# Optimization experiments

Hardware: AMD Instinct MI355X
Metric: run time of the kernel (lower is better)

The kernel has to match this reference:

```python
import jax, jax.numpy as jnp
import numpy as np

B, C, K, H, W = 64, 512, 64, 64, 64
EPS = 1e-12  # torch F.normalize eps


def setup_inputs() -> dict:
    key = jax.random.key(0)
    k1, k2, k3, k4 = jax.random.split(key, 4)
    x = jax.random.normal(k1, (B, C, H, W), dtype=jnp.float32)
    conv_w = jax.random.normal(k2, (K, C), dtype=jnp.float32) * 0.1  # 1x1 conv weight, squeezed
    conv_b = jax.random.normal(k3, (K,), dtype=jnp.float32) * 0.1
    centroids = jax.random.normal(k4, (K, C), dtype=jnp.float32)
    return {"x": x, "conv_w": conv_w, "conv_b": conv_b, "centroids": centroids}


def _l2norm(v, axis):
    n = jnp.sqrt(jnp.sum(v * v, axis=axis, keepdims=True))
    return v / jnp.maximum(n, EPS)


def reference(x, conv_w, conv_b, centroids):
    b, c, h, w = x.shape
    k = centroids.shape[0]
    hw = h * w
    # F.normalize(x, p=2, dim=1)
    xn = _l2norm(x, axis=1)
    # 1x1 conv -> [b,k,h,w] -> [b,k,hw], softmax over clusters
    logits = jnp.einsum('bchw,kc->bkhw', xn, conv_w) + conv_b[None, :, None, None]
    soft_assign = jax.nn.softmax(logits.reshape(b, k, hw), axis=1)
    # faithful to original: x.view(b, -1, c) with NO permute (channel-major reinterpretation)
    x_flatten = xn.reshape(b, hw, c)
    # vlad[b,k,c] = sum_i a[b,k,i] * (xf[b,i,c] - cent[k,c])
    vlad = (jnp.einsum('bki,bic->bkc', soft_assign, x_flatten)
            - jnp.sum(soft_assign, axis=2)[:, :, None] * centroids[None])
    vlad = _l2norm(vlad, axis=2)            # intra-normalize per cluster
    vlad = vlad.reshape(b, -1)
    vlad = _l2norm(vlad, axis=1)            # global L2 normalize
    return vlad
```

## Files before the change

kernel.cpp:

```cpp
#include <hip/hip_runtime.h>

#define HW 4096
#define NC 512
#define NK 64
#define NB 64

typedef unsigned short u16;
typedef float  float4v __attribute__((ext_vector_type(4)));
typedef short  short8  __attribute__((ext_vector_type(8)));

__device__ __forceinline__ u16 f2bf(float f){
  unsigned u = __builtin_bit_cast(unsigned, f);
  u += 0x7fffu + ((u >> 16) & 1u);
  return (u16)(u >> 16);
}
__device__ __forceinline__ unsigned pk2(float a, float b){
  return (unsigned)f2bf(a) | ((unsigned)f2bf(b) << 16);
}

__global__ __launch_bounds__(256) void nv_k1(
    const float* __restrict__ x, const float* __restrict__ w,
    const float* __restrict__ bias, float* __restrict__ invnorm,
    u16* __restrict__ a_out, float* __restrict__ asum)
{
  __shared__ u16 w_sh[NK * 40];
  __shared__ u16 x_sh[256 * 40];
  __shared__ float bias_sh[NK];

  const int t    = threadIdx.x;
  const int b    = blockIdx.y;
  const int p0   = blockIdx.x * 256;
  const int wave = t >> 6, lane = t & 63, q = lane >> 4, l16 = lane & 15;

  if (t < NK) bias_sh[t] = bias[t];

  const float* xb = x + (size_t)b * NC * HW;
  float sumsq = 0.f;

  float4v acc[4][4];
  const float4v zf = {0.f, 0.f, 0.f, 0.f};
  #pragma unroll
  for (int i = 0; i < 4; ++i)
    #pragma unroll
    for (int j = 0; j < 4; ++j) acc[i][j] = zf;

  for (int step = 0; step < 16; ++step){
    const int c0 = step * 32;
    __syncthreads();
    {
      const int m = t >> 2, cq = (t & 3) * 8;
      const float* wp = w + m * NC + c0 + cq;
      float4 w0 = *(const float4*)wp;
      float4 w1 = *(const float4*)(wp + 4);
      uint4 pk;
      pk.x = pk2(w0.x, w0.y); pk.y = pk2(w0.z, w0.w);
      pk.z = pk2(w1.x, w1.y); pk.w = pk2(w1.z, w1.w);
      *(uint4*)&w_sh[m * 40 + cq] = pk;
    }
    {
      const float* xp = xb + (size_t)c0 * HW + p0 + t;
      #pragma unroll
      for (int c8 = 0; c8 < 4; ++c8){
        float v0 = xp[(c8*8+0)*HW], v1 = xp[(c8*8+1)*HW];
        float v2 = xp[(c8*8+2)*HW], v3 = xp[(c8*8+3)*HW];
        float v4 = xp[(c8*8+4)*HW], v5 = xp[(c8*8+5)*HW];
        float v6 = xp[(c8*8+6)*HW], v7 = xp[(c8*8+7)*HW];
        sumsq += v0*v0 + v1*v1 + v2*v2 + v3*v3 + v4*v4 + v5*v5 + v6*v6 + v7*v7;
        uint4 pk;
        pk.x = pk2(v0, v1); pk.y = pk2(v2, v3);
        pk.z = pk2(v4, v5); pk.w = pk2(v6, v7);
        *(uint4*)&x_sh[t * 40 + c8 * 8] = pk;
      }
    }
    __syncthreads();
    short8 av[4], bv[4];
    #pragma unroll
    for (int ms = 0; ms < 4; ++ms)
      av[ms] = *(const short8*)&w_sh[(ms*16 + l16) * 40 + q*8];
    #pragma unroll
    for (int ns = 0; ns < 4; ++ns)
      bv[ns] = *(const short8*)&x_sh[(wave*64 + ns*16 + l16) * 40 + q*8];
    #pragma unroll
    for (int ms = 0; ms < 4; ++ms)
      #pragma unroll
      for (int ns = 0; ns < 4; ++ns)
        acc[ms][ns] = __builtin_amdgcn_mfma_f32_16x16x32_bf16(av[ms], bv[ns], acc[ms][ns], 0, 0, 0);
  }

  float inv = 1.f / fmaxf(sqrtf(sumsq), 1e-12f);
  invnorm[(size_t)b * HW + p0 + t] = inv;

  float inv_n[4];
  #pragma unroll
  for (int ns = 0; ns < 4; ++ns) inv_n[ns] = __shfl(inv, ns*16 + l16, 64);

  #pragma unroll
  for (int ns = 0; ns < 4; ++ns){
    float mx = -3.4e38f;
    #pragma unroll
    for (int ms = 0; ms < 4; ++ms)
      #pragma unroll
      for (int r = 0; r < 4; ++r){
        float lv = fmaf(acc[ms][ns][r], inv_n[ns], bias_sh[ms*16 + q*4 + r]);
        acc[ms][ns][r] = lv;
        mx = fmaxf(mx, lv);
      }
    mx = fmaxf(mx, __shfl_xor(mx, 16, 64));
    mx = fmaxf(mx, __shfl_xor(mx, 32, 64));
    float s = 0.f;
    #pragma unroll
    for (int ms = 0; ms < 4; ++ms)
      #pragma unroll
      for (int r = 0; r < 4; ++r){
        float e = __expf(acc[ms][ns][r] - mx);
        acc[ms][ns][r] = e;
        s += e;
      }
    s += __shfl_xor(s, 16, 64);
    s += __shfl_xor(s, 32, 64);
    float is = 1.f / s;
    #pragma unroll
    for (int ms = 0; ms < 4; ++ms)
      #pragma unroll
      for (int r = 0; r < 4; ++r) acc[ms][ns][r] *= is;
  }

  u16* ap = a_out + (size_t)b * NK * HW + p0 + wave * 64;
  #pragma unroll
  for (int ms = 0; ms < 4; ++ms)
    #pragma unroll
    for (int r = 0; r < 4; ++r){
      const int m = ms*16 + q*4 + r;
      #pragma unroll
      for (int ns = 0; ns < 4; ++ns)
        ap[(size_t)m * HW + ns*16 + l16] = f2bf(acc[ms][ns][r]);
    }

  #pragma unroll
  for (int ms = 0; ms < 4; ++ms)
    #pragma unroll
    for (int r = 0; r < 4; ++r){
      const int m = ms*16 + q*4 + r;
      float s = acc[ms][0][r] + acc[ms][1][r] + acc[ms][2][r] + acc[ms][3][r];
      s += __shfl_xor(s, 1, 64); s += __shfl_xor(s, 2, 64);
      s += __shfl_xor(s, 4, 64); s += __shfl_xor(s, 8, 64);
      if (l16 == 0) atomicAdd(&asum[b * NK + m], s);
    }
}

__global__ __launch_bounds__(256) void nv_k2(
    const float* __restrict__ x, const u16* __restrict__ a_buf,
    const float* __restrict__ invnorm, const float* __restrict__ asum,
    const float* __restrict__ cent, float* __restrict__ vlad)
{
  __shared__ u16 a_sh[NK * 40];
  __shared__ u16 x_sh[32 * 132];
  __shared__ float inv_sh[8 * 128];
  __shared__ float asum_sh[NK];

  const int t    = threadIdx.x;
  const int b    = blockIdx.y;
  const int cc0  = blockIdx.x * 128;
  const int wave = t >> 6, lane = t & 63, q = lane >> 4, l16 = lane & 15;

  {
    const int r = t >> 5, ccl = (t & 31) * 4;
    *(float4*)&inv_sh[r * 128 + ccl] =
        *(const float4*)&invnorm[(size_t)b * HW + r * NC + cc0 + ccl];
  }
  if (t < NK) asum_sh[t] = asum[b * NK + t];
  __syncthreads();

  const int il = t >> 5, cc_off = (t & 31) * 4;
  const float4 iv = *(const float4*)&inv_sh[il * 128 + cc_off];

  const float* xb = x + (size_t)b * NC * HW;
  const u16*   ab = a_buf + (size_t)b * NK * HW;

  float4v acc[4][2];
  const float4v zf = {0.f, 0.f, 0.f, 0.f};
  #pragma unroll
  for (int i = 0; i < 4; ++i){ acc[i][0] = zf; acc[i][1] = zf; }

  for (int step = 0; step < 128; ++step){
    const int i0 = step * 32;
    __syncthreads();
    {
      const int k = t >> 2, iq = (t & 3) * 8;
      *(float4*)&a_sh[k * 40 + iq] = *(const float4*)&ab[(size_t)k * HW + i0 + iq];
    }
    #pragma unroll
    for (int rr = 0; rr < 4; ++rr){
      const int i = i0 + il + rr * 8;
      const float* xp = xb + (size_t)i * NC + cc0 + cc_off;
      float4 xv = *(const float4*)xp;
      uint2 pk;
      pk.x = pk2(xv.x * iv.x, xv.y * iv.y);
      pk.y = pk2(xv.z * iv.z, xv.w * iv.w);
      *(uint2*)&x_sh[(il + rr * 8) * 132 + cc_off] = pk;
    }
    __syncthreads();
    short8 av[4];
    #pragma unroll
    for (int ms = 0; ms < 4; ++ms)
      av[ms] = *(const short8*)&a_sh[(ms*16 + l16) * 40 + q*8];
    #pragma unroll
    for (int ns = 0; ns < 2; ++ns){
      const int nn = wave * 32 + ns * 16 + l16;
      short8 bv;
      #pragma unroll
      for (int j = 0; j < 8; ++j)
        bv[j] = (short)x_sh[(q*8 + j) * 132 + nn];
      #pragma unroll
      for (int ms = 0; ms < 4; ++ms)
        acc[ms][ns] = __builtin_amdgcn_mfma_f32_16x16x32_bf16(av[ms], bv, acc[ms][ns], 0, 0, 0);
    }
  }

  #pragma unroll
  for (int ms = 0; ms < 4; ++ms)
    #pragma unroll
    for (int ns = 0; ns < 2; ++ns)
      #pragma unroll
      for (int r = 0; r < 4; ++r){
        const int m = ms*16 + q*4 + r;
        const int n = cc0 + wave*32 + ns*16 + l16;
        float v = acc[ms][ns][r] - asum_sh[m] * cent[m * NC + n];
        vlad[(size_t)(b * NK + m) * NC + n] = v;
      }
}

__global__ __launch_bounds__(256) void nv_k3(
    const float* __restrict__ vlad, float* __restrict__ out)
{
  __shared__ float part[256];
  __shared__ float rinv[NK];
  __shared__ float gsh[NK];
  __shared__ float gscale;

  const int b = blockIdx.x, t = threadIdx.x;
  const float* vb = vlad + (size_t)b * NK * NC;

  const int k = t >> 2, seg = t & 3;
  const float* vr = vb + k * NC + seg * 128;
  float s = 0.f;
  #pragma unroll 8
  for (int j = 0; j < 32; ++j){
    float4 v = *(const float4*)&vr[j * 4];
    s += v.x*v.x + v.y*v.y + v.z*v.z + v.w*v.w;
  }
  part[t] = s;
  __syncthreads();
  if (t < NK){
    float rs = part[t*4] + part[t*4+1] + part[t*4+2] + part[t*4+3];
    float ri = 1.f / fmaxf(sqrtf(rs), 1e-12f);
    rinv[t] = ri;
    gsh[t]  = rs * ri * ri;
  }
  __syncthreads();
  if (t == 0){
    float g = 0.f;
    for (int i = 0; i < NK; ++i) g += gsh[i];
    gscale = 1.f / fmaxf(sqrtf(g), 1e-12f);
  }
  __syncthreads();
  const float gv = gscale;
  float* ob = out + (size_t)b * NK * NC;
  for (int j = 0; j < 32; ++j){
    const int idx = j * 1024 + t * 4;
    float4 v = *(const float4*)&vb[idx];
    float sc = rinv[idx >> 9] * gv;
    float4 o; o.x = v.x*sc; o.y = v.y*sc; o.z = v.z*sc; o.w = v.w*sc;
    *(float4*)&ob[idx] = o;
  }
}

extern "C" void kernel_launch(void* const* d_in, const int* in_sizes, int n_in,
                              void* d_out, int out_size, void* d_ws, size_t ws_size,
                              hipStream_t stream)
{
  (void)in_sizes; (void)n_in; (void)out_size; (void)ws_size;
  const float* x    = (const float*)d_in[0];
  const float* w    = (const float*)d_in[1];
  const float* bias = (const float*)d_in[2];
  const float* cent = (const float*)d_in[3];
  float* out = (float*)d_out;

  char* ws = (char*)d_ws;
  float* invnorm = (float*)ws;
  u16*   a_buf   = (u16*)(ws + (1u << 20));
  float* asum    = (float*)(ws + (1u << 20) + (32u << 20));
  float* vlad    = (float*)(ws + (1u << 20) + (32u << 20) + 65536u);

  hipMemsetAsync(asum, 0, NB * NK * sizeof(float), stream);
  hipLaunchKernelGGL(nv_k1, dim3(16, 64), dim3(256), 0, stream,
                     x, w, bias, invnorm, a_buf, asum);
  hipLaunchKernelGGL(nv_k2, dim3(4, 64), dim3(256), 0, stream,
                     x, a_buf, invnorm, asum, cent, vlad);
  hipLaunchKernelGGL(nv_k3, dim3(64), dim3(256), 0, stream, vlad, out);
}
```

Baseline: 847.5 us.

## Split VLAD aggregation over spatial chunks and load x directly into registers

The aggregation kernel now splits the 4096 spatial positions into four chunks across a 3D grid and widens each block to 256 channels. Blocks write partial sums, which a new reduction kernel combines while also subtracting the centroid term and computing row norms. The x tile is loaded from global memory straight into MFMA B-operand registers with the inverse norms held in registers, replacing the LDS staging. This raises the grid from 256 to 512 blocks and cuts LDS traffic, at the cost of extra partial-buffer traffic, strided global loads and one more kernel launch.

```diff
diff --git a/kernel.cpp b/kernel.cpp
--- a/kernel.cpp
+++ b/kernel.cpp
@@ -150,126 +150,146 @@
 
 __global__ __launch_bounds__(256) void nv_k2(
     const float* __restrict__ x, const u16* __restrict__ a_buf,
-    const float* __restrict__ invnorm, const float* __restrict__ asum,
-    const float* __restrict__ cent, float* __restrict__ vlad)
+    const float* __restrict__ invnorm, float* __restrict__ vpart)
 {
   __shared__ u16 a_sh[NK * 40];
-  __shared__ u16 x_sh[32 * 132];
-  __shared__ float inv_sh[8 * 128];
-  __shared__ float asum_sh[NK];
 
   const int t    = threadIdx.x;
-  const int b    = blockIdx.y;
-  const int cc0  = blockIdx.x * 128;
+  const int b    = blockIdx.z;
+  const int iq   = blockIdx.y;
+  const int cc0  = blockIdx.x * 256;
   const int wave = t >> 6, lane = t & 63, q = lane >> 4, l16 = lane & 15;
 
-  {
-    const int r = t >> 5, ccl = (t & 31) * 4;
-    *(float4*)&inv_sh[r * 128 + ccl] =
-        *(const float4*)&invnorm[(size_t)b * HW + r * NC + cc0 + ccl];
-  }
-  if (t < NK) asum_sh[t] = asum[b * NK + t];
-  __syncthreads();
-
-  const int il = t >> 5, cc_off = (t & 31) * 4;
-  const float4 iv = *(const float4*)&inv_sh[il * 128 + cc_off];
-
-  const float* xb = x + (size_t)b * NC * HW;
-  const u16*   ab = a_buf + (size_t)b * NK * HW;
-
-  float4v acc[4][2];
+  const int cbase = cc0 + wave * 64 + l16;
+
+  const float* invb = invnorm + (size_t)b * HW;
+  float invr[4][8];
+  #pragma unroll
+  for (int ns = 0; ns < 4; ++ns)
+    #pragma unroll
+    for (int j = 0; j < 8; ++j)
+      invr[ns][j] = invb[j * 512 + cbase + ns * 16];
+
+  const float* xb  = x + (size_t)b * NC * HW;
+  const u16*   ab  = a_buf + (size_t)b * NK * HW + iq * 1024;
+  const float* xpb = xb + (size_t)(iq * 128 + q) * HW + cbase;
+
+  float4v acc[4][4];
   const float4v zf = {0.f, 0.f, 0.f, 0.f};
   #pragma unroll
-  for (int i = 0; i < 4; ++i){ acc[i][0] = zf; acc[i][1] = zf; }
-
-  for (int step = 0; step < 128; ++step){
+  for (int i = 0; i < 4; ++i)
+    #pragma unroll
+    for (int j = 0; j < 4; ++j) acc[i][j] = zf;
+
+  for (int step = 0; step < 32; ++step){
     const int i0 = step * 32;
     __syncthreads();
     {
-      const int k = t >> 2, iq = (t & 3) * 8;
-      *(float4*)&a_sh[k * 40 + iq] = *(const float4*)&ab[(size_t)k * HW + i0 + iq];
-    }
-    #pragma unroll
-    for (int rr = 0; rr < 4; ++rr){
-      const int i = i0 + il + rr * 8;
-      const float* xp = xb + (size_t)i * NC + cc0 + cc_off;
-      float4 xv = *(const float4*)xp;
-      uint2 pk;
-      pk.x = pk2(xv.x * iv.x, xv.y * iv.y);
-      pk.y = pk2(xv.z * iv.z, xv.w * iv.w);
-      *(uint2*)&x_sh[(il + rr * 8) * 132 + cc_off] = pk;
+      const int k = t >> 2, i8 = (t & 3) * 8;
+      *(float4*)&a_sh[k * 40 + i8] = *(const float4*)&ab[(size_t)k * HW + i0 + i8];
     }
     __syncthreads();
     short8 av[4];
     #pragma unroll
     for (int ms = 0; ms < 4; ++ms)
       av[ms] = *(const short8*)&a_sh[(ms*16 + l16) * 40 + q*8];
-    #pragma unroll
-    for (int ns = 0; ns < 2; ++ns){
-      const int nn = wave * 32 + ns * 16 + l16;
+
+    const float* xs = xpb + (size_t)step * 4 * HW;
+    #pragma unroll
+    for (int ns = 0; ns < 4; ++ns){
+      float v[8];
+      #pragma unroll
+      for (int j = 0; j < 8; ++j)
+        v[j] = xs[j * 512 + ns * 16] * invr[ns][j];
       short8 bv;
       #pragma unroll
-      for (int j = 0; j < 8; ++j)
-        bv[j] = (short)x_sh[(q*8 + j) * 132 + nn];
+      for (int j = 0; j < 4; ++j)
+        ((unsigned*)&bv)[j] = pk2(v[2*j], v[2*j+1]);
       #pragma unroll
       for (int ms = 0; ms < 4; ++ms)
         acc[ms][ns] = __builtin_amdgcn_mfma_f32_16x16x32_bf16(av[ms], bv, acc[ms][ns], 0, 0, 0);
     }
   }
 
+  float* vp = vpart + (size_t)(iq * NB + b) * NK * NC;
   #pragma unroll
   for (int ms = 0; ms < 4; ++ms)
     #pragma unroll
-    for (int ns = 0; ns < 2; ++ns)
+    for (int ns = 0; ns < 4; ++ns)
       #pragma unroll
       for (int r = 0; r < 4; ++r){
         const int m = ms*16 + q*4 + r;
-        const int n = cc0 + wave*32 + ns*16 + l16;
-        float v = acc[ms][ns][r] - asum_sh[m] * cent[m * NC + n];
-        vlad[(size_t)(b * NK + m) * NC + n] = v;
+        const int n = cc0 + wave*64 + ns*16 + l16;
+        vp[(size_t)m * NC + n] = acc[ms][ns][r];
       }
 }
 
-__global__ __launch_bounds__(256) void nv_k3(
-    const float* __restrict__ vlad, float* __restrict__ out)
-{
-  __shared__ float part[256];
-  __shared__ float rinv[NK];
-  __shared__ float gsh[NK];
-  __shared__ float gscale;
-
+__global__ __launch_bounds__(256) void nv_k3a(
+    const float* __restrict__ vpart, const float* __restrict__ asum,
+    const float* __restrict__ cent, float* __restrict__ vlad,
+    float* __restrict__ rstat)
+{
+  __shared__ float part_sh[256];
   const int b = blockIdx.x, t = threadIdx.x;
-  const float* vb = vlad + (size_t)b * NK * NC;
-
   const int k = t >> 2, seg = t & 3;
-  const float* vr = vb + k * NC + seg * 128;
+  const size_t roff = ((size_t)b * NK + k) * NC + seg * 128;
+  const size_t bstride = (size_t)NB * NK * NC;
+  const float* p0 = vpart + roff;
+  const float as = asum[b * NK + k];
+  const float* cp = cent + k * NC + seg * 128;
+  float* vp = vlad + roff;
+
   float s = 0.f;
-  #pragma unroll 8
+  #pragma unroll 4
   for (int j = 0; j < 32; ++j){
-    float4 v = *(const float4*)&vr[j * 4];
+    float4 a0 = *(const float4*)&p0[j*4];
+    float4 a1 = *(const float4*)&p0[bstride + j*4];
+    float4 a2 = *(const float4*)&p0[2*bstride + j*4];
+    float4 a3 = *(const float4*)&p0[3*bstride + j*4];
+    float4 c4 = *(const float4*)&cp[j*4];
+    float4 v;
+    v.x = (a0.x + a1.x) + (a2.x + a3.x) - as * c4.x;
+    v.y = (a0.y + a1.y) + (a2.y + a3.y) - as * c4.y;
+    v.z = (a0.z + a1.z) + (a2.z + a3.z) - as * c4.z;
+    v.w = (a0.w + a1.w) + (a2.w + a3.w) - as * c4.w;
+    *(float4*)&vp[j*4] = v;
     s += v.x*v.x + v.y*v.y + v.z*v.z + v.w*v.w;
   }
-  part[t] = s;
+  part_sh[t] = s;
   __syncthreads();
   if (t < NK){
-    float rs = part[t*4] + part[t*4+1] + part[t*4+2] + part[t*4+3];
+    float rs = part_sh[t*4] + part_sh[t*4+1] + part_sh[t*4+2] + part_sh[t*4+3];
     float ri = 1.f / fmaxf(sqrtf(rs), 1e-12f);
-    rinv[t] = ri;
-    gsh[t]  = rs * ri * ri;
+    rstat[b * 128 + t]      = ri;
+    rstat[b * 128 + 64 + t] = rs * ri * ri;
+  }
+}
+
+__global__ __launch_bounds__(256) void nv_k3c(
+    const float* __restrict__ vlad, const float* __restrict__ rstat,
+    float* __restrict__ out)
+{
+  __shared__ float rinv_sh[NK];
+  __shared__ float gsh;
+  const int b = blockIdx.x, t = threadIdx.x;
+  if (t < 64){
+    float ri = rstat[b * 128 + t];
+    rinv_sh[t] = ri;
+    float sk = rstat[b * 128 + 64 + t];
+    sk += __shfl_xor(sk, 1, 64);  sk += __shfl_xor(sk, 2, 64);
+    sk += __shfl_xor(sk, 4, 64);  sk += __shfl_xor(sk, 8, 64);
+    sk += __shfl_xor(sk, 16, 64); sk += __shfl_xor(sk, 32, 64);
+    if (t == 0) gsh = 1.f / fmaxf(sqrtf(sk), 1e-12f);
   }
   __syncthreads();
-  if (t == 0){
-    float g = 0.f;
-    for (int i = 0; i < NK; ++i) g += gsh[i];
-    gscale = 1.f / fmaxf(sqrtf(g), 1e-12f);
-  }
-  __syncthreads();
-  const float gv = gscale;
+  const float g = gsh;
+  const float* vb = vlad + (size_t)b * NK * NC;
   float* ob = out + (size_t)b * NK * NC;
+  #pragma unroll 4
   for (int j = 0; j < 32; ++j){
     const int idx = j * 1024 + t * 4;
     float4 v = *(const float4*)&vb[idx];
-    float sc = rinv[idx >> 9] * gv;
+    float sc = rinv_sh[idx >> 9] * g;
     float4 o; o.x = v.x*sc; o.y = v.y*sc; o.z = v.z*sc; o.w = v.w*sc;
     *(float4*)&ob[idx] = o;
   }
@@ -288,14 +308,19 @@
 
   char* ws = (char*)d_ws;
   float* invnorm = (float*)ws;
-  u16*   a_buf   = (u16*)(ws + (1u << 20));
-  float* asum    = (float*)(ws + (1u << 20) + (32u << 20));
-  float* vlad    = (float*)(ws + (1u << 20) + (32u << 20) + 65536u);
+  u16*   a_buf   = (u16*)(ws + (1u  << 20));
+  float* asum    = (float*)(ws + (33u << 20));
+  float* rstat   = (float*)(ws + (33u << 20) + 65536u);
+  float* vlad    = (float*)(ws + (34u << 20));
+  float* vpart   = (float*)(ws + (42u << 20));
 
   hipMemsetAsync(asum, 0, NB * NK * sizeof(float), stream);
   hipLaunchKernelGGL(nv_k1, dim3(16, 64), dim3(256), 0, stream,
                      x, w, bias, invnorm, a_buf, asum);
-  hipLaunchKernelGGL(nv_k2, dim3(4, 64), dim3(256), 0, stream,
-                     x, a_buf, invnorm, asum, cent, vlad);
-  hipLaunchKernelGGL(nv_k3, dim3(64), dim3(256), 0, stream, vlad, out);
-}
+  hipLaunchKernelGGL(nv_k2, dim3(2, 4, 64), dim3(256), 0, stream,
+                     x, a_buf, invnorm, vpart);
+  hipLaunchKernelGGL(nv_k3a, dim3(64), dim3(256), 0, stream,
+                     vpart, asum, cent, vlad, rstat);
+  hipLaunchKernelGGL(nv_k3c, dim3(64), dim3(256), 0, stream,
+                     vlad, rstat, out);
+}
```

Measured after the change: 836.1 us. Within noise of the previous version (-1.3%).
